# Kernel optimization log

Measured on AMD Instinct MI355X. Metric: run time of the kernel, lower is better.

The kernel has to match this reference:

```python
import jax, jax.numpy as jnp
import numpy as np


def setup_inputs() -> dict:
    key = jax.random.key(0)
    kq, kk, kv = jax.random.split(key, 3)
    B, H, N, D = 2, 16, 4096, 128
    return {
        "query": jax.random.normal(kq, (B, H, N, D), dtype=jnp.float32),
        "key": jax.random.normal(kk, (B, H, N, D), dtype=jnp.float32),
        "value": jax.random.normal(kv, (B, H, N, D), dtype=jnp.float32),
        "n_query_groups": 4,
        "n_key_groups": 4,
        "k_picked": 0,  # deterministic stand-in for random.randint(0, n_gp[1]-1)
    }


def _kronecker_attention(query, key, value, m, n, k_picked):
    """Kronecker-factorized attention: A ~= S_{m x n} kron B_{p x q}.

    B is exact attention of the center query group vs center key group;
    S is estimated from sampled q.k scores via per-group L2 norms; groups are
    merged with numerically-stable online LSE combination.
    """
    b, h, nq, d = query.shape
    nk = key.shape[2]
    scale = 1.0 / jnp.sqrt(jnp.asarray(d, query.dtype))
    p, q = nq // m, nk // n          # tokens per query / key group
    c0, c1 = m // 2, n // 2          # center groups

    # --- exact attention on center block, against ALL value groups at once ---
    q_gp = query[:, :, c0 * p:(c0 + 1) * p, :]            # (b,h,p,d)
    k_gp = key[:, :, c1 * q:(c1 + 1) * q, :]              # (b,h,q,d)
    # value.chunk(n, dim=-2) then cat(dim=-1): (b,h,q,n*d), feature block j = value group j
    v_gp = jnp.moveaxis(value.reshape(b, h, n, q, d), 2, 3).reshape(b, h, q, n * d)
    scores = jnp.einsum('bhpd,bhqd->bhpq', q_gp, k_gp) * scale
    lse0 = jax.scipy.special.logsumexp(scores, axis=-1)   # (b,h,p)
    probs = jnp.exp(scores - lse0[..., None])
    attn_gp = jnp.einsum('bhpq,bhqe->bhpe', probs, v_gp)  # (b,h,p,n*d)
    attn_blocks = jnp.moveaxis(attn_gp.reshape(b, h, p, n, d), 3, 2)  # (b,h,n,p,d)

    # --- group-scale estimation: one sampled key per key group ---
    k_sample = key[:, :, k_picked::q, :]                  # (b,h,n,d)
    w = jnp.einsum('bhld,bhgd->bhlg', query, k_sample)    # (b,h,nq,n)
    norms = jnp.linalg.norm(w.reshape(b, h, m, p, n), axis=3)  # (b,h,m,n)
    s = norms / norms[:, :, c0, c1][:, :, None, None]     # normalized by center group

    # --- vectorized stable LSE merge across key groups, per query group ---
    # scaled attention matrix s*A -> lse shifts by log(s); outputs stay normalized
    lse_ij = lse0[:, :, None, :, None] + jnp.log(s)[:, :, :, None, :]  # (b,h,m,p,n)
    lse_m = jax.scipy.special.logsumexp(lse_ij, axis=-1)               # (b,h,m,p)
    wts = jnp.exp(lse_ij - lse_m[..., None])                           # (b,h,m,p,n)
    attn = jnp.einsum('bhmpn,bhnpd->bhmpd', wts, attn_blocks).reshape(b, h, nq, d)
    lse = lse_m.reshape(b, h, nq, 1)
    return attn, lse


def reference(query, key, value, n_query_groups, n_key_groups, k_picked):
    return _kronecker_attention(query, key, value, n_query_groups, n_key_groups, k_picked)
```

## Files before the change

kernel.cpp:

```cpp
#include <hip/hip_runtime.h>


typedef _Float16 f16x8 __attribute__((ext_vector_type(8)));
typedef _Float16 f16x4 __attribute__((ext_vector_type(4)));
typedef float    f32x4 __attribute__((ext_vector_type(4)));

#define SCALE 0.08838834764831845f

__device__ __forceinline__ int xcd_swz(int wg, int nwg) {
  int chunk = nwg >> 3;
  return (wg & 7) * chunk + (wg >> 3);
}

__global__ __launch_bounds__(256) void k_build_kc(const float* __restrict__ k,
                                                  _Float16* __restrict__ Kc) {
  int idx = blockIdx.x * 256 + threadIdx.x;
  int bh  = idx >> 15;
  int rem = idx & 32767;
  int r   = rem >> 5, c4 = rem & 31;
  float4 v = *(const float4*)(k + ((size_t)bh * 4096 + 2048 + r) * 128 + c4 * 4);
  f16x4 o = {(_Float16)v.x, (_Float16)v.y, (_Float16)v.z, (_Float16)v.w};
  *(f16x4*)(Kc + ((size_t)bh * 1024 + r) * 128 + c4 * 4) = o;
}

__global__ __launch_bounds__(256) void k_build_vt(const float* __restrict__ v,
                                                  _Float16* __restrict__ VT) {
  __shared__ _Float16 tile[128 * 136];
  int blk = blockIdx.x;
  int bh = blk >> 5, g = (blk >> 3) & 3, kt = blk & 7;
  int t = threadIdx.x;
  const float* src = v + ((size_t)bh * 4096 + g * 1024 + kt * 128) * 128;
#pragma unroll
  for (int i = 0; i < 16; ++i) {
    int idx = i * 256 + t;
    int r = idx >> 5, c4 = idx & 31;
    float4 vv = *(const float4*)(src + (size_t)r * 128 + c4 * 4);
    f16x4 o = {(_Float16)vv.x, (_Float16)vv.y, (_Float16)vv.z, (_Float16)vv.w};
    *(f16x4*)&tile[r * 136 + c4 * 4] = o;
  }
  __syncthreads();
  _Float16* dst = VT + (size_t)(bh * 4 + g) * 128 * 1024 + kt * 128;
#pragma unroll
  for (int i = 0; i < 16; ++i) {
    int idx = i * 256 + t;
    int dd = idx >> 5, k4 = idx & 31;
    f16x4 o = {tile[(k4 * 4 + 0) * 136 + dd], tile[(k4 * 4 + 1) * 136 + dd],
               tile[(k4 * 4 + 2) * 136 + dd], tile[(k4 * 4 + 3) * 136 + dd]};
    *(f16x4*)(dst + (size_t)dd * 1024 + k4 * 4) = o;
  }
}

__global__ __launch_bounds__(256) void k_norms(const float* __restrict__ q,
                                               const float* __restrict__ k,
                                               float* __restrict__ norms2) {
  __shared__ float ks[4][128];
  int b = blockIdx.x;
  int bh = b >> 4, qi = (b >> 2) & 3, sl = b & 3;
  int t = threadIdx.x;
  for (int i = t; i < 512; i += 256)
    ks[i >> 7][i & 127] = k[((size_t)bh * 4096 + (i >> 7) * 1024) * 128 + (i & 127)];
  __syncthreads();
  int w = t >> 6, lane = t & 63, l15 = lane & 15, l4 = lane >> 4;
  float ksr[4][8];
#pragma unroll
  for (int gg = 0; gg < 4; ++gg)
#pragma unroll
    for (int j = 0; j < 8; ++j) ksr[gg][j] = ks[gg][l15 * 8 + j];
  float n2[4] = {0.f, 0.f, 0.f, 0.f};
  const float* qb = q + ((size_t)bh * 4096 + qi * 1024 + sl * 256) * 128;
  for (int it = 0; it < 16; ++it) {
    int row = it * 16 + w * 4 + l4;
    const float* qr = qb + (size_t)row * 128 + l15 * 8;
    float4 qa = *(const float4*)qr;
    float4 qc = *(const float4*)(qr + 4);
#pragma unroll
    for (int gg = 0; gg < 4; ++gg) {
      float p = qa.x * ksr[gg][0] + qa.y * ksr[gg][1] + qa.z * ksr[gg][2] +
                qa.w * ksr[gg][3] + qc.x * ksr[gg][4] + qc.y * ksr[gg][5] +
                qc.z * ksr[gg][6] + qc.w * ksr[gg][7];
      p += __shfl_xor(p, 1); p += __shfl_xor(p, 2);
      p += __shfl_xor(p, 4); p += __shfl_xor(p, 8);
      if (l15 == 0) n2[gg] += p * p;
    }
  }
  if (l15 == 0) {
#pragma unroll
    for (int gg = 0; gg < 4; ++gg)
      atomicAdd(&norms2[bh * 16 + qi * 4 + gg], n2[gg]);
  }
}

__global__ void k_wts(const float* __restrict__ norms2, float* __restrict__ wts,
                      float* __restrict__ logS) {
  int t = threadIdx.x;
  if (t < 128) {
    int bh = t >> 2, qi = t & 3;
    float n0 = sqrtf(norms2[bh * 16 + qi * 4 + 0]);
    float n1 = sqrtf(norms2[bh * 16 + qi * 4 + 1]);
    float n2v = sqrtf(norms2[bh * 16 + qi * 4 + 2]);
    float n3 = sqrtf(norms2[bh * 16 + qi * 4 + 3]);
    float S = n0 + n1 + n2v + n3;
    float nc = sqrtf(norms2[bh * 16 + 2 * 4 + 2]);
    float inv = 1.f / S;
    wts[bh * 16 + qi * 4 + 0] = n0 * inv;
    wts[bh * 16 + qi * 4 + 1] = n1 * inv;
    wts[bh * 16 + qi * 4 + 2] = n2v * inv;
    wts[bh * 16 + qi * 4 + 3] = n3 * inv;
    logS[bh * 4 + qi] = __logf(S) - __logf(nc);
  }
}

__global__ __launch_bounds__(512, 4) void k_lse0(const float* __restrict__ q,
                                                 const _Float16* __restrict__ Kc,
                                                 float* __restrict__ lse0) {
  __shared__ _Float16 Qt[128 * 136];
  __shared__ _Float16 Kt[64 * 136];
  int wg = xcd_swz(blockIdx.x, 256);
  int bh = wg >> 3;
  int q0 = (wg & 7) << 7;
  int t = threadIdx.x;
  int w = t >> 6, lane = t & 63, l15 = lane & 15, l4 = lane >> 4;
  const float* qbase = q + ((size_t)bh * 4096 + 2048 + q0) * 128;
#pragma unroll
  for (int i = 0; i < 8; ++i) {
    int idx = i * 512 + t;
    int r = idx >> 5, c4 = idx & 31;
    float4 vv = *(const float4*)(qbase + (size_t)r * 128 + c4 * 4);
    f16x4 o = {(_Float16)vv.x, (_Float16)vv.y, (_Float16)vv.z, (_Float16)vv.w};
    *(f16x4*)&Qt[r * 136 + c4 * 4] = o;
  }
  float m[4] = {-1e30f, -1e30f, -1e30f, -1e30f};
  float lsum[4] = {0.f, 0.f, 0.f, 0.f};
  const _Float16* kc_b = Kc + (size_t)bh * 1024 * 128;
  for (int kt = 0; kt < 16; ++kt) {
    __syncthreads();
#pragma unroll
    for (int i = 0; i < 2; ++i) {
      int idx = i * 512 + t;
      int r = idx >> 4, c8 = idx & 15;
      *(uint4*)&Kt[r * 136 + c8 * 8] =
          *(const uint4*)(kc_b + ((size_t)kt * 64 + r) * 128 + c8 * 8);
    }
    __syncthreads();
    f32x4 z = {0.f, 0.f, 0.f, 0.f};
    f32x4 sv0 = z, sv1 = z, sv2 = z, sv3 = z;
#pragma unroll
    for (int ks = 0; ks < 4; ++ks) {
      f16x8 a  = *(const f16x8*)&Qt[(w * 16 + l15) * 136 + ks * 32 + l4 * 8];
      f16x8 b0 = *(const f16x8*)&Kt[(0 + l15) * 136 + ks * 32 + l4 * 8];
      f16x8 b1 = *(const f16x8*)&Kt[(16 + l15) * 136 + ks * 32 + l4 * 8];
      f16x8 b2 = *(const f16x8*)&Kt[(32 + l15) * 136 + ks * 32 + l4 * 8];
      f16x8 b3 = *(const f16x8*)&Kt[(48 + l15) * 136 + ks * 32 + l4 * 8];
      sv0 = __builtin_amdgcn_mfma_f32_16x16x32_f16(a, b0, sv0, 0, 0, 0);
      sv1 = __builtin_amdgcn_mfma_f32_16x16x32_f16(a, b1, sv1, 0, 0, 0);
      sv2 = __builtin_amdgcn_mfma_f32_16x16x32_f16(a, b2, sv2, 0, 0, 0);
      sv3 = __builtin_amdgcn_mfma_f32_16x16x32_f16(a, b3, sv3, 0, 0, 0);
    }
#pragma unroll
    for (int r = 0; r < 4; ++r) {
      float v0 = sv0[r] * SCALE, v1 = sv1[r] * SCALE;
      float v2 = sv2[r] * SCALE, v3 = sv3[r] * SCALE;
      float vm = fmaxf(fmaxf(v0, v1), fmaxf(v2, v3));
      vm = fmaxf(vm, __shfl_xor(vm, 1));
      vm = fmaxf(vm, __shfl_xor(vm, 2));
      vm = fmaxf(vm, __shfl_xor(vm, 4));
      vm = fmaxf(vm, __shfl_xor(vm, 8));
      float mn = fmaxf(m[r], vm);
      float ps = __expf(v0 - mn) + __expf(v1 - mn) + __expf(v2 - mn) + __expf(v3 - mn);
      ps += __shfl_xor(ps, 1); ps += __shfl_xor(ps, 2);
      ps += __shfl_xor(ps, 4); ps += __shfl_xor(ps, 8);
      lsum[r] = lsum[r] * __expf(m[r] - mn) + ps;
      m[r] = mn;
    }
  }
  if (l15 == 0) {
#pragma unroll
    for (int r = 0; r < 4; ++r) {
      int row = w * 16 + l4 * 4 + r;
      lse0[bh * 1024 + q0 + row] = m[r] + __logf(lsum[r]);
    }
  }
}

#define SMEM_MAIN 118080
__global__ __launch_bounds__(512, 2) void k_main(
    const float* __restrict__ q, const _Float16* __restrict__ Kc,
    const _Float16* __restrict__ VT, const float* __restrict__ lse0,
    const float* __restrict__ wtsg, const float* __restrict__ logSg,
    float* __restrict__ out) {
  extern __shared__ char smem[];
  _Float16* Qt = (_Float16*)smem;
  _Float16* Kt = (_Float16*)(smem + 17408);
  _Float16* Pt = (_Float16*)(smem + 34816);
  _Float16* Vt = (_Float16*)(smem + 44032);
  float* lse_t = (float*)(smem + 117760);
  float* wts_t = (float*)(smem + 118016);
  float* Ag    = (float*)(smem + 44032);

  int wg = xcd_swz(blockIdx.x, 512);
  int bh = wg >> 4;
  int q0 = (wg & 15) << 6;
  int t = threadIdx.x;
  int w = t >> 6, lane = t & 63, l15 = lane & 15, l4 = lane >> 4;
  int g = w >> 1, dh = w & 1;
  int sr0 = (w & 3) * 16, sc0 = (w >> 2) * 32;

  const float* qbase = q + ((size_t)bh * 4096 + 2048 + q0) * 128;
#pragma unroll
  for (int i = 0; i < 4; ++i) {
    int idx = i * 512 + t;
    int r = idx >> 5, c4 = idx & 31;
    float4 vv = *(const float4*)(qbase + (size_t)r * 128 + c4 * 4);
    f16x4 o = {(_Float16)vv.x, (_Float16)vv.y, (_Float16)vv.z, (_Float16)vv.w};
    *(f16x4*)&Qt[r * 136 + c4 * 4] = o;
  }
  if (t < 64) lse_t[t] = lse0[bh * 1024 + q0 + t];
  if (t < 16) wts_t[t] = wtsg[bh * 16 + t];

  f32x4 z = {0.f, 0.f, 0.f, 0.f};
  f32x4 acc[4][4];
#pragma unroll
  for (int i = 0; i < 4; ++i)
#pragma unroll
    for (int j = 0; j < 4; ++j) acc[i][j] = z;

  const _Float16* kc_b = Kc + (size_t)bh * 1024 * 128;
  const _Float16* vt_b = VT + (size_t)bh * 4 * 128 * 1024;

  for (int kt = 0; kt < 16; ++kt) {
    __syncthreads();
#pragma unroll
    for (int i = 0; i < 2; ++i) {
      int idx = i * 512 + t;
      int r = idx >> 4, c8 = idx & 15;
      *(uint4*)&Kt[r * 136 + c8 * 8] =
          *(const uint4*)(kc_b + ((size_t)kt * 64 + r) * 128 + c8 * 8);
    }
#pragma unroll
    for (int i = 0; i < 8; ++i) {
      int idx = i * 512 + t;
      int row = idx >> 3, c8 = idx & 7;
      *(uint4*)&Vt[row * 72 + c8 * 8] =
          *(const uint4*)(vt_b + (size_t)row * 1024 + kt * 64 + c8 * 8);
    }
    __syncthreads();
    f32x4 sv0 = z, sv1 = z;
#pragma unroll
    for (int ks = 0; ks < 4; ++ks) {
      f16x8 a  = *(const f16x8*)&Qt[(sr0 + l15) * 136 + ks * 32 + l4 * 8];
      f16x8 b0 = *(const f16x8*)&Kt[(sc0 + l15) * 136 + ks * 32 + l4 * 8];
      f16x8 b1 = *(const f16x8*)&Kt[(sc0 + 16 + l15) * 136 + ks * 32 + l4 * 8];
      sv0 = __builtin_amdgcn_mfma_f32_16x16x32_f16(a, b0, sv0, 0, 0, 0);
      sv1 = __builtin_amdgcn_mfma_f32_16x16x32_f16(a, b1, sv1, 0, 0, 0);
    }
#pragma unroll
    for (int r = 0; r < 4; ++r) {
      int row = sr0 + l4 * 4 + r;
      float ls = lse_t[row];
      Pt[row * 72 + sc0 + l15]      = (_Float16)__expf(sv0[r] * SCALE - ls);
      Pt[row * 72 + sc0 + 16 + l15] = (_Float16)__expf(sv1[r] * SCALE - ls);
    }
    __syncthreads();
#pragma unroll
    for (int ks = 0; ks < 2; ++ks) {
      f16x8 bf[4];
#pragma unroll
      for (int ct = 0; ct < 4; ++ct)
        bf[ct] = *(const f16x8*)&Vt[(g * 128 + dh * 64 + ct * 16 + l15) * 72 +
                                    ks * 32 + l4 * 8];
#pragma unroll
      for (int rt = 0; rt < 4; ++rt) {
        f16x8 a = *(const f16x8*)&Pt[(rt * 16 + l15) * 72 + ks * 32 + l4 * 8];
#pragma unroll
        for (int ct = 0; ct < 4; ++ct)
          acc[rt][ct] = __builtin_amdgcn_mfma_f32_16x16x32_f16(a, bf[ct], acc[rt][ct], 0, 0, 0);
      }
    }
  }
  __syncthreads();
  if (g < 2) {
#pragma unroll
    for (int rt = 0; rt < 4; ++rt)
#pragma unroll
      for (int ct = 0; ct < 4; ++ct)
#pragma unroll
        for (int r = 0; r < 4; ++r)
          Ag[g * 8192 + (rt * 16 + l4 * 4 + r) * 128 + dh * 64 + ct * 16 + l15] =
              acc[rt][ct][r];
  }
  __syncthreads();
  float part[4][16];
#pragma unroll
  for (int i = 0; i < 16; ++i) {
    int e = i * 512 + t;
    int r = e >> 7, c = e & 127;
    float a0 = Ag[r * 128 + c], a1 = Ag[8192 + r * 128 + c];
#pragma unroll
    for (int qi = 0; qi < 4; ++qi)
      part[qi][i] = wts_t[qi * 4 + 0] * a0 + wts_t[qi * 4 + 1] * a1;
  }
  __syncthreads();
  if (g >= 2) {
#pragma unroll
    for (int rt = 0; rt < 4; ++rt)
#pragma unroll
      for (int ct = 0; ct < 4; ++ct)
#pragma unroll
        for (int r = 0; r < 4; ++r)
          Ag[(g - 2) * 8192 + (rt * 16 + l4 * 4 + r) * 128 + dh * 64 + ct * 16 + l15] =
              acc[rt][ct][r];
  }
  __syncthreads();
  float* obase = out + ((size_t)bh * 4096 + q0) * 128;
#pragma unroll
  for (int i = 0; i < 16; ++i) {
    int e = i * 512 + t;
    int r = e >> 7, c = e & 127;
    float a2 = Ag[r * 128 + c], a3 = Ag[8192 + r * 128 + c];
#pragma unroll
    for (int qi = 0; qi < 4; ++qi) {
      float val = part[qi][i] + wts_t[qi * 4 + 2] * a2 + wts_t[qi * 4 + 3] * a3;
      obase[(size_t)(qi * 1024 + r) * 128 + c] = val;
    }
  }
  if (t < 256) {
    int qi = t >> 6, r = t & 63;
    out[16777216 + (size_t)bh * 4096 + qi * 1024 + q0 + r] = lse_t[r] + logSg[bh * 4 + qi];
  }
}

#define VT_OFF   0u
#define LSE0_OFF 33554432u
#define N2_OFF   33685504u
#define WTS_OFF  33687552u
#define LOGS_OFF 33689600u
#define KC_OFF   33690112u
#define WS_NEED  42078720u

extern "C" void kernel_launch(void* const* d_in, const int* in_sizes, int n_in,
                              void* d_out, int out_size, void* d_ws, size_t ws_size,
                              hipStream_t stream) {
  const float* q = (const float*)d_in[0];
  const float* k = (const float*)d_in[1];
  const float* v = (const float*)d_in[2];
  float* out = (float*)d_out;
  char* ws = (char*)d_ws;
  if (ws_size < WS_NEED) return;

  _Float16* VT   = (_Float16*)(ws + VT_OFF);
  float* lse0    = (float*)(ws + LSE0_OFF);
  float* norms2  = (float*)(ws + N2_OFF);
  float* wtsb    = (float*)(ws + WTS_OFF);
  float* logSb   = (float*)(ws + LOGS_OFF);
  _Float16* Kc   = (_Float16*)(ws + KC_OFF);

  hipFuncSetAttribute(reinterpret_cast<const void*>(k_main),
                      hipFuncAttributeMaxDynamicSharedMemorySize, SMEM_MAIN);

  hipMemsetAsync(norms2, 0, 2048, stream);
  k_build_kc<<<4096, 256, 0, stream>>>(k, Kc);
  k_build_vt<<<1024, 256, 0, stream>>>(v, VT);
  k_norms<<<512, 256, 0, stream>>>(q, k, norms2);
  k_wts<<<1, 128, 0, stream>>>(norms2, wtsb, logSb);
  k_lse0<<<256, 512, 0, stream>>>(q, Kc, lse0);
  k_main<<<512, 512, SMEM_MAIN, stream>>>(q, Kc, VT, lse0, wtsb, logSb, out);
}
```

Before: 391.3 us.

## Fuse lse0 pass into main kernel with online softmax and direct-global K/V operands

Removes the separate k_lse0 kernel and computes the row max and sum inside k_main with an online-softmax rescale of the accumulators, cross-wave max exchange through shared memory, and a ballot flag that skips rescaling when no max changes. K and V fragments are now loaded straight from global memory into MFMA operands instead of staged through LDS. Q and P tiles use an XOR swizzle in place of padding, and the epilogue writes normalized fp16 partials in two phases. The goal is to avoid recomputing QK^T twice and to cut LDS so three workgroups fit per CU, at the cost of extra barriers per tile and uncoalesced global operand loads.

```diff
diff --git a/kernel.cpp b/kernel.cpp
--- a/kernel.cpp
+++ b/kernel.cpp
@@ -25,7 +25,7 @@
 
 __global__ __launch_bounds__(256) void k_build_vt(const float* __restrict__ v,
                                                   _Float16* __restrict__ VT) {
-  __shared__ _Float16 tile[128 * 136];
+  __shared__ _Float16 tile[128 * 132];
   int blk = blockIdx.x;
   int bh = blk >> 5, g = (blk >> 3) & 3, kt = blk & 7;
   int t = threadIdx.x;
@@ -36,7 +36,7 @@
     int r = idx >> 5, c4 = idx & 31;
     float4 vv = *(const float4*)(src + (size_t)r * 128 + c4 * 4);
     f16x4 o = {(_Float16)vv.x, (_Float16)vv.y, (_Float16)vv.z, (_Float16)vv.w};
-    *(f16x4*)&tile[r * 136 + c4 * 4] = o;
+    *(f16x4*)&tile[r * 132 + c4 * 4] = o;
   }
   __syncthreads();
   _Float16* dst = VT + (size_t)(bh * 4 + g) * 128 * 1024 + kt * 128;
@@ -44,8 +44,8 @@
   for (int i = 0; i < 16; ++i) {
     int idx = i * 256 + t;
     int dd = idx >> 5, k4 = idx & 31;
-    f16x4 o = {tile[(k4 * 4 + 0) * 136 + dd], tile[(k4 * 4 + 1) * 136 + dd],
-               tile[(k4 * 4 + 2) * 136 + dd], tile[(k4 * 4 + 3) * 136 + dd]};
+    f16x4 o = {tile[(k4 * 4 + 0) * 132 + dd], tile[(k4 * 4 + 1) * 132 + dd],
+               tile[(k4 * 4 + 2) * 132 + dd], tile[(k4 * 4 + 3) * 132 + dd]};
     *(f16x4*)(dst + (size_t)dd * 1024 + k4 * 4) = o;
   }
 }
@@ -110,92 +110,30 @@
   }
 }
 
-__global__ __launch_bounds__(512, 4) void k_lse0(const float* __restrict__ q,
-                                                 const _Float16* __restrict__ Kc,
-                                                 float* __restrict__ lse0) {
-  __shared__ _Float16 Qt[128 * 136];
-  __shared__ _Float16 Kt[64 * 136];
-  int wg = xcd_swz(blockIdx.x, 256);
-  int bh = wg >> 3;
-  int q0 = (wg & 7) << 7;
-  int t = threadIdx.x;
-  int w = t >> 6, lane = t & 63, l15 = lane & 15, l4 = lane >> 4;
-  const float* qbase = q + ((size_t)bh * 4096 + 2048 + q0) * 128;
-#pragma unroll
-  for (int i = 0; i < 8; ++i) {
-    int idx = i * 512 + t;
-    int r = idx >> 5, c4 = idx & 31;
-    float4 vv = *(const float4*)(qbase + (size_t)r * 128 + c4 * 4);
-    f16x4 o = {(_Float16)vv.x, (_Float16)vv.y, (_Float16)vv.z, (_Float16)vv.w};
-    *(f16x4*)&Qt[r * 136 + c4 * 4] = o;
-  }
-  float m[4] = {-1e30f, -1e30f, -1e30f, -1e30f};
-  float lsum[4] = {0.f, 0.f, 0.f, 0.f};
-  const _Float16* kc_b = Kc + (size_t)bh * 1024 * 128;
-  for (int kt = 0; kt < 16; ++kt) {
-    __syncthreads();
-#pragma unroll
-    for (int i = 0; i < 2; ++i) {
-      int idx = i * 512 + t;
-      int r = idx >> 4, c8 = idx & 15;
-      *(uint4*)&Kt[r * 136 + c8 * 8] =
-          *(const uint4*)(kc_b + ((size_t)kt * 64 + r) * 128 + c8 * 8);
-    }
-    __syncthreads();
-    f32x4 z = {0.f, 0.f, 0.f, 0.f};
-    f32x4 sv0 = z, sv1 = z, sv2 = z, sv3 = z;
-#pragma unroll
-    for (int ks = 0; ks < 4; ++ks) {
-      f16x8 a  = *(const f16x8*)&Qt[(w * 16 + l15) * 136 + ks * 32 + l4 * 8];
-      f16x8 b0 = *(const f16x8*)&Kt[(0 + l15) * 136 + ks * 32 + l4 * 8];
-      f16x8 b1 = *(const f16x8*)&Kt[(16 + l15) * 136 + ks * 32 + l4 * 8];
-      f16x8 b2 = *(const f16x8*)&Kt[(32 + l15) * 136 + ks * 32 + l4 * 8];
-      f16x8 b3 = *(const f16x8*)&Kt[(48 + l15) * 136 + ks * 32 + l4 * 8];
-      sv0 = __builtin_amdgcn_mfma_f32_16x16x32_f16(a, b0, sv0, 0, 0, 0);
-      sv1 = __builtin_amdgcn_mfma_f32_16x16x32_f16(a, b1, sv1, 0, 0, 0);
-      sv2 = __builtin_amdgcn_mfma_f32_16x16x32_f16(a, b2, sv2, 0, 0, 0);
-      sv3 = __builtin_amdgcn_mfma_f32_16x16x32_f16(a, b3, sv3, 0, 0, 0);
-    }
-#pragma unroll
-    for (int r = 0; r < 4; ++r) {
-      float v0 = sv0[r] * SCALE, v1 = sv1[r] * SCALE;
-      float v2 = sv2[r] * SCALE, v3 = sv3[r] * SCALE;
-      float vm = fmaxf(fmaxf(v0, v1), fmaxf(v2, v3));
-      vm = fmaxf(vm, __shfl_xor(vm, 1));
-      vm = fmaxf(vm, __shfl_xor(vm, 2));
-      vm = fmaxf(vm, __shfl_xor(vm, 4));
-      vm = fmaxf(vm, __shfl_xor(vm, 8));
-      float mn = fmaxf(m[r], vm);
-      float ps = __expf(v0 - mn) + __expf(v1 - mn) + __expf(v2 - mn) + __expf(v3 - mn);
-      ps += __shfl_xor(ps, 1); ps += __shfl_xor(ps, 2);
-      ps += __shfl_xor(ps, 4); ps += __shfl_xor(ps, 8);
-      lsum[r] = lsum[r] * __expf(m[r] - mn) + ps;
-      m[r] = mn;
-    }
-  }
-  if (l15 == 0) {
-#pragma unroll
-    for (int r = 0; r < 4; ++r) {
-      int row = w * 16 + l4 * 4 + r;
-      lse0[bh * 1024 + q0 + row] = m[r] + __logf(lsum[r]);
-    }
-  }
-}
-
-#define SMEM_MAIN 118080
-__global__ __launch_bounds__(512, 2) void k_main(
+#define QT_OFF 0
+#define PT_OFF 16384
+#define ST_OFF 32768
+#define PMAX_OFF (ST_OFF + 0)
+#define PSW_OFF  (ST_OFF + 512)
+#define RSC_OFF  (ST_OFF + 1024)
+#define FLG_OFF  (ST_OFF + 1280)
+#define LINV_OFF (ST_OFF + 1296)
+#define LSEV_OFF (ST_OFF + 1552)
+#define WTS2_OFF (ST_OFF + 1808)
+#define SMEM_SZ  (ST_OFF + 1872)
+
+__global__ __launch_bounds__(512, 3) void k_main(
     const float* __restrict__ q, const _Float16* __restrict__ Kc,
-    const _Float16* __restrict__ VT, const float* __restrict__ lse0,
-    const float* __restrict__ wtsg, const float* __restrict__ logSg,
-    float* __restrict__ out) {
-  extern __shared__ char smem[];
-  _Float16* Qt = (_Float16*)smem;
-  _Float16* Kt = (_Float16*)(smem + 17408);
-  _Float16* Pt = (_Float16*)(smem + 34816);
-  _Float16* Vt = (_Float16*)(smem + 44032);
-  float* lse_t = (float*)(smem + 117760);
-  float* wts_t = (float*)(smem + 118016);
-  float* Ag    = (float*)(smem + 44032);
+    const _Float16* __restrict__ VT, const float* __restrict__ wtsg,
+    const float* __restrict__ logSg, float* __restrict__ out) {
+  __shared__ char smem[SMEM_SZ];
+  float* pmaxS = (float*)(smem + PMAX_OFF);
+  float* pswS  = (float*)(smem + PSW_OFF);
+  float* rscS  = (float*)(smem + RSC_OFF);
+  int*   flgS  = (int*)(smem + FLG_OFF);
+  float* linvS = (float*)(smem + LINV_OFF);
+  float* lseS  = (float*)(smem + LSEV_OFF);
+  float* wtsS  = (float*)(smem + WTS2_OFF);
 
   int wg = xcd_swz(blockIdx.x, 512);
   int bh = wg >> 4;
@@ -203,7 +141,8 @@
   int t = threadIdx.x;
   int w = t >> 6, lane = t & 63, l15 = lane & 15, l4 = lane >> 4;
   int g = w >> 1, dh = w & 1;
-  int sr0 = (w & 3) * 16, sc0 = (w >> 2) * 32;
+  int rb = w & 3, ch = w >> 2;
+  int sr0 = rb * 16, sc0 = ch * 32;
 
   const float* qbase = q + ((size_t)bh * 4096 + 2048 + q0) * 128;
 #pragma unroll
@@ -212,10 +151,10 @@
     int r = idx >> 5, c4 = idx & 31;
     float4 vv = *(const float4*)(qbase + (size_t)r * 128 + c4 * 4);
     f16x4 o = {(_Float16)vv.x, (_Float16)vv.y, (_Float16)vv.z, (_Float16)vv.w};
-    *(f16x4*)&Qt[r * 136 + c4 * 4] = o;
-  }
-  if (t < 64) lse_t[t] = lse0[bh * 1024 + q0 + t];
-  if (t < 16) wts_t[t] = wtsg[bh * 16 + t];
+    *(f16x4*)(smem + QT_OFF + r * 256 + ((c4 * 8) ^ ((r & 7) << 4))) = o;
+  }
+  if (t < 16) wtsS[t] = wtsg[bh * 16 + t];
+  __syncthreads();
 
   f32x4 z = {0.f, 0.f, 0.f, 0.f};
   f32x4 acc[4][4];
@@ -223,119 +162,172 @@
   for (int i = 0; i < 4; ++i)
 #pragma unroll
     for (int j = 0; j < 4; ++j) acc[i][j] = z;
-
-  const _Float16* kc_b = Kc + (size_t)bh * 1024 * 128;
-  const _Float16* vt_b = VT + (size_t)bh * 4 * 128 * 1024;
+  float m_[4] = {-1e30f, -1e30f, -1e30f, -1e30f};
+  float l_[4] = {0.f, 0.f, 0.f, 0.f};
+
+  const _Float16* kp = Kc + (size_t)bh * 131072 + (size_t)(sc0 + l15) * 128 + l4 * 8;
+  const _Float16* vp = VT + (size_t)bh * 524288 +
+                       (size_t)(g * 128 + dh * 64 + l15) * 1024 + l4 * 8;
 
   for (int kt = 0; kt < 16; ++kt) {
-    __syncthreads();
-#pragma unroll
-    for (int i = 0; i < 2; ++i) {
-      int idx = i * 512 + t;
-      int r = idx >> 4, c8 = idx & 15;
-      *(uint4*)&Kt[r * 136 + c8 * 8] =
-          *(const uint4*)(kc_b + ((size_t)kt * 64 + r) * 128 + c8 * 8);
-    }
-#pragma unroll
-    for (int i = 0; i < 8; ++i) {
-      int idx = i * 512 + t;
-      int row = idx >> 3, c8 = idx & 7;
-      *(uint4*)&Vt[row * 72 + c8 * 8] =
-          *(const uint4*)(vt_b + (size_t)row * 1024 + kt * 64 + c8 * 8);
-    }
-    __syncthreads();
     f32x4 sv0 = z, sv1 = z;
+    const _Float16* kpt = kp + kt * 8192;
 #pragma unroll
     for (int ks = 0; ks < 4; ++ks) {
-      f16x8 a  = *(const f16x8*)&Qt[(sr0 + l15) * 136 + ks * 32 + l4 * 8];
-      f16x8 b0 = *(const f16x8*)&Kt[(sc0 + l15) * 136 + ks * 32 + l4 * 8];
-      f16x8 b1 = *(const f16x8*)&Kt[(sc0 + 16 + l15) * 136 + ks * 32 + l4 * 8];
+      int qrow = sr0 + l15;
+      f16x8 a = *(const f16x8*)(smem + QT_OFF + qrow * 256 +
+                                ((ks * 64 + l4 * 16) ^ ((qrow & 7) << 4)));
+      f16x8 b0 = *(const f16x8*)(kpt + ks * 32);
+      f16x8 b1 = *(const f16x8*)(kpt + 2048 + ks * 32);
       sv0 = __builtin_amdgcn_mfma_f32_16x16x32_f16(a, b0, sv0, 0, 0, 0);
       sv1 = __builtin_amdgcn_mfma_f32_16x16x32_f16(a, b1, sv1, 0, 0, 0);
     }
+    float pm[4];
+#pragma unroll
+    for (int r = 0; r < 4; ++r) {
+      sv0[r] *= SCALE; sv1[r] *= SCALE;
+      float p = fmaxf(sv0[r], sv1[r]);
+      p = fmaxf(p, __shfl_xor(p, 1));
+      p = fmaxf(p, __shfl_xor(p, 2));
+      p = fmaxf(p, __shfl_xor(p, 4));
+      p = fmaxf(p, __shfl_xor(p, 8));
+      pm[r] = p;
+    }
+    if (l15 == 0) {
+#pragma unroll
+      for (int r = 0; r < 4; ++r) pmaxS[ch * 64 + sr0 + l4 * 4 + r] = pm[r];
+    }
+    __syncthreads();
+    float mnew[4];
+    bool chg = false;
 #pragma unroll
     for (int r = 0; r < 4; ++r) {
       int row = sr0 + l4 * 4 + r;
-      float ls = lse_t[row];
-      Pt[row * 72 + sc0 + l15]      = (_Float16)__expf(sv0[r] * SCALE - ls);
-      Pt[row * 72 + sc0 + 16 + l15] = (_Float16)__expf(sv1[r] * SCALE - ls);
-    }
-    __syncthreads();
+      float pb = fmaxf(pmaxS[row], pmaxS[64 + row]);
+      mnew[r] = fmaxf(m_[r], pb);
+      chg = chg || (mnew[r] > m_[r]);
+    }
+    if (ch == 0) {
+      if (l15 == 0) {
+#pragma unroll
+        for (int r = 0; r < 4; ++r)
+          rscS[sr0 + l4 * 4 + r] = __expf(m_[r] - mnew[r]);
+      }
+      unsigned long long bal = __ballot(chg);
+      if (lane == 0) flgS[rb] = (bal != 0ull) ? 1 : 0;
+    }
+#pragma unroll
+    for (int r = 0; r < 4; ++r) {
+      int row = sr0 + l4 * 4 + r;
+      float p0 = __expf(sv0[r] - mnew[r]);
+      float p1 = __expf(sv1[r] - mnew[r]);
+      int rswz = (row & 7) << 4;
+      *(_Float16*)(smem + PT_OFF + row * 128 + (((sc0 + l15) * 2) ^ rswz)) =
+          (_Float16)p0;
+      *(_Float16*)(smem + PT_OFF + row * 128 + (((sc0 + 16 + l15) * 2) ^ rswz)) =
+          (_Float16)p1;
+      float ps = p0 + p1;
+      ps += __shfl_xor(ps, 1); ps += __shfl_xor(ps, 2);
+      ps += __shfl_xor(ps, 4); ps += __shfl_xor(ps, 8);
+      if (l15 == 0) pswS[ch * 64 + row] = ps;
+    }
+    __syncthreads();
+    int anyf = flgS[0] | flgS[1] | flgS[2] | flgS[3];
+#pragma unroll
+    for (int r = 0; r < 4; ++r) {
+      int row = sr0 + l4 * 4 + r;
+      l_[r] = l_[r] * rscS[row] + pswS[row] + pswS[64 + row];
+      m_[r] = mnew[r];
+    }
+    if (anyf) {
+#pragma unroll
+      for (int rt = 0; rt < 4; ++rt)
+#pragma unroll
+        for (int rr = 0; rr < 4; ++rr) {
+          float rsv = rscS[rt * 16 + l4 * 4 + rr];
+#pragma unroll
+          for (int ct = 0; ct < 4; ++ct) acc[rt][ct][rr] *= rsv;
+        }
+    }
+    const _Float16* vpt = vp + kt * 64;
 #pragma unroll
     for (int ks = 0; ks < 2; ++ks) {
       f16x8 bf[4];
 #pragma unroll
       for (int ct = 0; ct < 4; ++ct)
-        bf[ct] = *(const f16x8*)&Vt[(g * 128 + dh * 64 + ct * 16 + l15) * 72 +
-                                    ks * 32 + l4 * 8];
+        bf[ct] = *(const f16x8*)(vpt + (size_t)ct * 16384 + ks * 32);
 #pragma unroll
       for (int rt = 0; rt < 4; ++rt) {
-        f16x8 a = *(const f16x8*)&Pt[(rt * 16 + l15) * 72 + ks * 32 + l4 * 8];
+        int arow = rt * 16 + l15;
+        f16x8 a = *(const f16x8*)(smem + PT_OFF + arow * 128 +
+                                  ((ks * 64 + l4 * 16) ^ ((arow & 7) << 4)));
 #pragma unroll
         for (int ct = 0; ct < 4; ++ct)
-          acc[rt][ct] = __builtin_amdgcn_mfma_f32_16x16x32_f16(a, bf[ct], acc[rt][ct], 0, 0, 0);
+          acc[rt][ct] =
+              __builtin_amdgcn_mfma_f32_16x16x32_f16(a, bf[ct], acc[rt][ct], 0, 0, 0);
       }
     }
+    __syncthreads();
+  }
+
+  if (ch == 0 && l15 == 0) {
+#pragma unroll
+    for (int r = 0; r < 4; ++r) {
+      int row = sr0 + l4 * 4 + r;
+      linvS[row] = 1.0f / l_[r];
+      lseS[row] = m_[r] + __logf(l_[r]);
+    }
   }
   __syncthreads();
-  if (g < 2) {
-#pragma unroll
-    for (int rt = 0; rt < 4; ++rt)
-#pragma unroll
-      for (int ct = 0; ct < 4; ++ct)
-#pragma unroll
-        for (int r = 0; r < 4; ++r)
-          Ag[g * 8192 + (rt * 16 + l4 * 4 + r) * 128 + dh * 64 + ct * 16 + l15] =
-              acc[rt][ct][r];
-  }
-  __syncthreads();
-  float part[4][16];
-#pragma unroll
-  for (int i = 0; i < 16; ++i) {
-    int e = i * 512 + t;
-    int r = e >> 7, c = e & 127;
-    float a0 = Ag[r * 128 + c], a1 = Ag[8192 + r * 128 + c];
-#pragma unroll
-    for (int qi = 0; qi < 4; ++qi)
-      part[qi][i] = wts_t[qi * 4 + 0] * a0 + wts_t[qi * 4 + 1] * a1;
-  }
-  __syncthreads();
-  if (g >= 2) {
-#pragma unroll
-    for (int rt = 0; rt < 4; ++rt)
-#pragma unroll
-      for (int ct = 0; ct < 4; ++ct)
-#pragma unroll
-        for (int r = 0; r < 4; ++r)
-          Ag[(g - 2) * 8192 + (rt * 16 + l4 * 4 + r) * 128 + dh * 64 + ct * 16 + l15] =
-              acc[rt][ct][r];
-  }
-  __syncthreads();
+
+  _Float16* AgS = (_Float16*)smem;
   float* obase = out + ((size_t)bh * 4096 + q0) * 128;
 #pragma unroll
-  for (int i = 0; i < 16; ++i) {
-    int e = i * 512 + t;
-    int r = e >> 7, c = e & 127;
-    float a2 = Ag[r * 128 + c], a3 = Ag[8192 + r * 128 + c];
-#pragma unroll
-    for (int qi = 0; qi < 4; ++qi) {
-      float val = part[qi][i] + wts_t[qi * 4 + 2] * a2 + wts_t[qi * 4 + 3] * a3;
-      obase[(size_t)(qi * 1024 + r) * 128 + c] = val;
-    }
+  for (int phase = 0; phase < 2; ++phase) {
+    if (dh == phase) {
+#pragma unroll
+      for (int rt = 0; rt < 4; ++rt)
+#pragma unroll
+        for (int rr = 0; rr < 4; ++rr) {
+          int arow = rt * 16 + l4 * 4 + rr;
+          float li = linvS[arow];
+#pragma unroll
+          for (int ct = 0; ct < 4; ++ct)
+            AgS[(g * 64 + arow) * 64 + ct * 16 + l15] =
+                (_Float16)(acc[rt][ct][rr] * li);
+        }
+    }
+    __syncthreads();
+#pragma unroll
+    for (int i = 0; i < 8; ++i) {
+      int e = i * 512 + t;
+      int rr = e >> 6, c = e & 63;
+      float a0 = (float)AgS[(0 * 64 + rr) * 64 + c];
+      float a1 = (float)AgS[(1 * 64 + rr) * 64 + c];
+      float a2 = (float)AgS[(2 * 64 + rr) * 64 + c];
+      float a3 = (float)AgS[(3 * 64 + rr) * 64 + c];
+#pragma unroll
+      for (int qi = 0; qi < 4; ++qi) {
+        float val = wtsS[qi * 4 + 0] * a0 + wtsS[qi * 4 + 1] * a1 +
+                    wtsS[qi * 4 + 2] * a2 + wtsS[qi * 4 + 3] * a3;
+        obase[(size_t)(qi * 1024 + rr) * 128 + phase * 64 + c] = val;
+      }
+    }
+    __syncthreads();
   }
   if (t < 256) {
-    int qi = t >> 6, r = t & 63;
-    out[16777216 + (size_t)bh * 4096 + qi * 1024 + q0 + r] = lse_t[r] + logSg[bh * 4 + qi];
+    int qi = t >> 6, rr = t & 63;
+    out[16777216 + (size_t)bh * 4096 + qi * 1024 + q0 + rr] =
+        lseS[rr] + logSg[bh * 4 + qi];
   }
 }
 
 #define VT_OFF   0u
-#define LSE0_OFF 33554432u
-#define N2_OFF   33685504u
-#define WTS_OFF  33687552u
-#define LOGS_OFF 33689600u
-#define KC_OFF   33690112u
-#define WS_NEED  42078720u
+#define KC_OFF   33554432u
+#define N2_OFF   41943040u
+#define WTSB_OFF 41945088u
+#define LOGS_OFF 41947136u
+#define WS_NEED  41947648u
 
 extern "C" void kernel_launch(void* const* d_in, const int* in_sizes, int n_in,
                               void* d_out, int out_size, void* d_ws, size_t ws_size,
@@ -348,20 +340,15 @@
   if (ws_size < WS_NEED) return;
 
   _Float16* VT   = (_Float16*)(ws + VT_OFF);
-  float* lse0    = (float*)(ws + LSE0_OFF);
+  _Float16* Kc   = (_Float16*)(ws + KC_OFF);
   float* norms2  = (float*)(ws + N2_OFF);
-  float* wtsb    = (float*)(ws + WTS_OFF);
+  float* wtsb    = (float*)(ws + WTSB_OFF);
   float* logSb   = (float*)(ws + LOGS_OFF);
-  _Float16* Kc   = (_Float16*)(ws + KC_OFF);
-
-  hipFuncSetAttribute(reinterpret_cast<const void*>(k_main),
-                      hipFuncAttributeMaxDynamicSharedMemorySize, SMEM_MAIN);
 
   hipMemsetAsync(norms2, 0, 2048, stream);
   k_build_kc<<<4096, 256, 0, stream>>>(k, Kc);
   k_build_vt<<<1024, 256, 0, stream>>>(v, VT);
   k_norms<<<512, 256, 0, stream>>>(q, k, norms2);
   k_wts<<<1, 128, 0, stream>>>(norms2, wtsb, logSb);
-  k_lse0<<<256, 512, 0, stream>>>(q, Kc, lse0);
-  k_main<<<512, 512, SMEM_MAIN, stream>>>(q, Kc, VT, lse0, wtsb, logSb, out);
-}
+  k_main<<<512, 512, 0, stream>>>(q, Kc, VT, wtsb, logSb, out);
+}
```

After: 419.1 us. 7.1% more time.
